# Optimization experiments

Measured on AMD Instinct MI355X. Metric: run time of the kernel, lower is better.

The kernel has to match this reference:

```python
import jax, jax.numpy as jnp
import numpy as np

EMB_DIM = 1024
NUM_HEADS = 16
HEAD_DIM = EMB_DIM // NUM_HEADS
B, S = 4, 2048


def setup_inputs() -> dict:
    key = jax.random.key(0)
    ks = jax.random.split(key, 16)
    def lin(k):
        return jax.random.normal(k, (EMB_DIM, EMB_DIM), jnp.float32) * (EMB_DIM ** -0.5)
    x = jax.random.normal(ks[0], (B, S, EMB_DIM), jnp.float32)
    positions = jnp.sort(jax.random.randint(ks[1], (B, S), 0, 100000), axis=-1)
    return {
        "x": x,
        "positions": positions,
        "Wq": lin(ks[2]), "bq": jnp.zeros((EMB_DIM,), jnp.float32),
        "Wk": lin(ks[3]), "bk": jnp.zeros((EMB_DIM,), jnp.float32),
        "Wv": lin(ks[4]), "bv": jnp.zeros((EMB_DIM,), jnp.float32),
        "Wo": lin(ks[5]), "bo": jnp.zeros((EMB_DIM,), jnp.float32),
        "q_scale": jnp.ones((EMB_DIM,), jnp.float32),
        "k_scale": jnp.ones((EMB_DIM,), jnp.float32),
        "v_scale": jnp.ones((EMB_DIM,), jnp.float32),
        "o_scale": jnp.ones((EMB_DIM,), jnp.float32),
    }


def _rotate(t, cos, sin):
    # t: (B, H, S, D); pairs of consecutive dims rotated by per-position angles.
    # cos/sin: (B, 1, S, D/2)
    tp = t.reshape(t.shape[:-1] + (HEAD_DIM // 2, 2))
    t0, t1 = tp[..., 0], tp[..., 1]
    r0 = t0 * cos - t1 * sin
    r1 = t0 * sin + t1 * cos
    return jnp.stack([r0, r1], axis=-1).reshape(t.shape)


def reference(x, positions, Wq, bq, Wk, bk, Wv, bv, Wo, bo,
              q_scale, k_scale, v_scale, o_scale):
    b, s, e = x.shape
    # theta_vector: standard RoPE inverse frequencies for head_dim
    theta = 1.0 / (10000.0 ** (jnp.arange(0, HEAD_DIM, 2, dtype=jnp.float32) / HEAD_DIM))
    angles = positions.astype(jnp.float32)[..., None] * theta  # (B, S, D/2)
    cos = jnp.cos(angles)[:, None, :, :]  # (B, 1, S, D/2)
    sin = jnp.sin(angles)[:, None, :, :]

    def proj(W, bias, scale):
        y = (x @ W + bias) * scale
        return y.reshape(b, s, NUM_HEADS, HEAD_DIM).transpose(0, 2, 1, 3)  # (B,H,S,D)

    Q = _rotate(proj(Wq, bq, q_scale), cos, sin)
    K = _rotate(proj(Wk, bk, k_scale), cos, sin)
    V = proj(Wv, bv, v_scale)

    scores = jnp.einsum('bhqd,bhkd->bhqk', Q, K) / jnp.sqrt(
        jnp.asarray(HEAD_DIM, jnp.float32))
    probs = jax.nn.softmax(scores, axis=-1)
    context = jnp.einsum('bhqk,bhkd->bhqd', probs, V)
    context = context.transpose(0, 2, 1, 3).reshape(b, s, e)
    return (context @ Wo + bo) * o_scale
```

## Files before the change

kernel.cpp:

```cpp
#include <hip/hip_runtime.h>
#include <hip/hip_bf16.h>

using bf16 = __hip_bfloat16;
typedef __attribute__((ext_vector_type(8))) short short8;
typedef __attribute__((ext_vector_type(4))) float f32x4;
typedef __attribute__((ext_vector_type(16))) float f32x16;

#define AS1 __attribute__((address_space(1)))
#define AS3 __attribute__((address_space(3)))

__device__ __forceinline__ void gload_lds16(const void* g, void* l) {
  __builtin_amdgcn_global_load_lds((const AS1 unsigned int*)g,
                                   (AS3 unsigned int*)l, 16, 0, 0);
}

__device__ __forceinline__ unsigned cvtpk_bf16(float lo, float hi) {
  unsigned r;
  asm("v_cvt_pk_bf16_f32 %0, %1, %2" : "=v"(r) : "v"(lo), "v"(hi));
  return r;
}

__device__ __forceinline__ void pl32swap(unsigned &a, unsigned &b) {
  asm("v_permlane32_swap_b32 %0, %1" : "+v"(a), "+v"(b));
}

__device__ __forceinline__ float fm3(float a, float b, float c) {
  return fmaxf(fmaxf(a, b), c);
}

__global__ __launch_bounds__(256) void k_convert(const float* __restrict__ src,
                                                 bf16* __restrict__ dst, int n4) {
  int i = blockIdx.x * 256 + threadIdx.x;
  if (i >= n4) return;
  float4 v = reinterpret_cast<const float4*>(src)[i];
  alignas(8) bf16 o[4] = {__float2bfloat16(v.x), __float2bfloat16(v.y),
                          __float2bfloat16(v.z), __float2bfloat16(v.w)};
  *reinterpret_cast<uint2*>(dst + (size_t)i * 4) = *reinterpret_cast<uint2*>(o);
}

__global__ __launch_bounds__(256) void k_wtrans(
    const float* __restrict__ W0, const float* __restrict__ W1,
    const float* __restrict__ W2, const float* __restrict__ W3,
    bf16* __restrict__ T0, bf16* __restrict__ T1,
    bf16* __restrict__ T2, bf16* __restrict__ T3) {
  __shared__ float tile[64][65];
  const float* W; bf16* T;
  switch (blockIdx.z) {
    case 0: W = W0; T = T0; break;
    case 1: W = W1; T = T1; break;
    case 2: W = W2; T = T2; break;
    default: W = W3; T = T3; break;
  }
  const int k0 = blockIdx.x * 64, n0 = blockIdx.y * 64;
  const int r = threadIdx.x >> 6, c = threadIdx.x & 63;
#pragma unroll
  for (int i = 0; i < 16; i++)
    tile[r + i * 4][c] = W[(size_t)(k0 + r + i * 4) * 1024 + n0 + c];
  __syncthreads();
#pragma unroll
  for (int i = 0; i < 16; i++)
    T[(size_t)(n0 + r + i * 4) * 1024 + k0 + c] = __float2bfloat16(tile[c][r + i * 4]);
}

__global__ __launch_bounds__(256) void k_gemm_qkv(
    const bf16* __restrict__ A, const bf16* __restrict__ BT,
    const float* __restrict__ bq, const float* __restrict__ bk,
    const float* __restrict__ bv, const float* __restrict__ sq,
    const float* __restrict__ sk, const float* __restrict__ sv,
    bf16* __restrict__ Yqkv) {
  __shared__ alignas(16) bf16 sA[128 * 32];
  __shared__ alignas(16) bf16 sB[128 * 32];
  const int K = 1024;
  const int lane = threadIdx.x & 63;
  const int wid = threadIdx.x >> 6;
  const int wr = wid >> 1, wc = wid & 1;
  const int m0 = blockIdx.x * 128;
  const int n0 = blockIdx.y * 128;

  f32x4 acc[4][4];
#pragma unroll
  for (int i = 0; i < 4; i++)
#pragma unroll
    for (int j = 0; j < 4; j++) acc[i][j] = f32x4{0.f, 0.f, 0.f, 0.f};

  const int srow = lane >> 2;
  const int scol = (lane & 3) * 8;

  for (int k0 = 0; k0 < K; k0 += 32) {
    __syncthreads();
#pragma unroll
    for (int cc = 0; cc < 2; cc++) {
      const int chunk = wid + cc * 4;
      gload_lds16(A + (size_t)(m0 + chunk * 16 + srow) * K + k0 + scol,
                  sA + chunk * 512);
      gload_lds16(BT + (size_t)(n0 + chunk * 16 + srow) * K + k0 + scol,
                  sB + chunk * 512);
    }
    __syncthreads();
    short8 af[4], bfr[4];
#pragma unroll
    for (int i = 0; i < 4; i++) {
      af[i] = *reinterpret_cast<const short8*>(
          sA + (wr * 64 + i * 16 + (lane & 15)) * 32 + (lane >> 4) * 8);
      bfr[i] = *reinterpret_cast<const short8*>(
          sB + (wc * 64 + i * 16 + (lane & 15)) * 32 + (lane >> 4) * 8);
    }
#pragma unroll
    for (int mi = 0; mi < 4; mi++)
#pragma unroll
      for (int ni = 0; ni < 4; ni++)
        acc[mi][ni] = __builtin_amdgcn_mfma_f32_16x16x32_bf16(
            af[mi], bfr[ni], acc[mi][ni], 0, 0, 0);
  }

  const int seg = n0 >> 10;
  bf16* dst = Yqkv + (size_t)seg * (8u << 20);
  const float* bias = seg == 0 ? bq : (seg == 1 ? bk : bv);
  const float* scale = seg == 0 ? sq : (seg == 1 ? sk : sv);
  const int nb = n0 & 1023;
#pragma unroll
  for (int ni = 0; ni < 4; ni++) {
    const int n = nb + wc * 64 + ni * 16 + (lane & 15);
    const float bz = bias[n];
    const float sc = scale[n];
#pragma unroll
    for (int mi = 0; mi < 4; mi++) {
      const int mr = m0 + wr * 64 + mi * 16 + (lane >> 4) * 4;
#pragma unroll
      for (int j = 0; j < 4; j++)
        dst[(size_t)(mr + j) * 1024 + n] = __float2bfloat16((acc[mi][ni][j] + bz) * sc);
    }
  }
}

__global__ __launch_bounds__(256) void k_gemm_bt(
    const bf16* __restrict__ A, const bf16* __restrict__ BT,
    const float* __restrict__ bias, const float* __restrict__ scale,
    float* __restrict__ Cout, int M, int N, int K) {
  __shared__ alignas(16) bf16 sA[128 * 32];
  __shared__ alignas(16) bf16 sB[128 * 32];
  const int lane = threadIdx.x & 63;
  const int wid = threadIdx.x >> 6;
  const int wr = wid >> 1, wc = wid & 1;
  const int m0 = blockIdx.x * 128;
  const int n0 = blockIdx.y * 128;

  f32x4 acc[4][4];
#pragma unroll
  for (int i = 0; i < 4; i++)
#pragma unroll
    for (int j = 0; j < 4; j++) acc[i][j] = f32x4{0.f, 0.f, 0.f, 0.f};

  const int srow = lane >> 2;
  const int scol = (lane & 3) * 8;

  for (int k0 = 0; k0 < K; k0 += 32) {
    __syncthreads();
#pragma unroll
    for (int cc = 0; cc < 2; cc++) {
      const int chunk = wid + cc * 4;
      gload_lds16(A + (size_t)(m0 + chunk * 16 + srow) * K + k0 + scol,
                  sA + chunk * 512);
      gload_lds16(BT + (size_t)(n0 + chunk * 16 + srow) * K + k0 + scol,
                  sB + chunk * 512);
    }
    __syncthreads();
    short8 af[4], bfr[4];
#pragma unroll
    for (int i = 0; i < 4; i++) {
      af[i] = *reinterpret_cast<const short8*>(
          sA + (wr * 64 + i * 16 + (lane & 15)) * 32 + (lane >> 4) * 8);
      bfr[i] = *reinterpret_cast<const short8*>(
          sB + (wc * 64 + i * 16 + (lane & 15)) * 32 + (lane >> 4) * 8);
    }
#pragma unroll
    for (int mi = 0; mi < 4; mi++)
#pragma unroll
      for (int ni = 0; ni < 4; ni++)
        acc[mi][ni] = __builtin_amdgcn_mfma_f32_16x16x32_bf16(
            af[mi], bfr[ni], acc[mi][ni], 0, 0, 0);
  }

#pragma unroll
  for (int ni = 0; ni < 4; ni++) {
    const int n = n0 + wc * 64 + ni * 16 + (lane & 15);
    const float bz = bias[n];
    const float sc = scale[n];
#pragma unroll
    for (int mi = 0; mi < 4; mi++) {
      const int mr = m0 + wr * 64 + mi * 16 + (lane >> 4) * 4;
#pragma unroll
      for (int j = 0; j < 4; j++)
        Cout[(size_t)(mr + j) * N + n] = (acc[mi][ni][j] + bz) * sc;
    }
  }
}

__global__ __launch_bounds__(256) void k_rope(const bf16* __restrict__ Y,
                                              const int* __restrict__ pos,
                                              bf16* __restrict__ Out, float mul) {
  const int idx = blockIdx.x * 256 + threadIdx.x;
  const int c = idx & 3;
  const int h = (idx >> 2) & 15;
  const int s = (idx >> 6) & 2047;
  const int b = idx >> 17;
  const float p = (float)pos[b * 2048 + s];
  const size_t ybase = ((size_t)(b * 2048 + s)) * 1024 + h * 64 + c * 16;
  const size_t obase = (((size_t)(b * 16 + h)) * 2048 + s) * 64 + c * 16;

  union { short8 v[2]; short a[16]; } in, out;
  in.v[0] = *reinterpret_cast<const short8*>(Y + ybase);
  in.v[1] = *reinterpret_cast<const short8*>(Y + ybase + 8);
#pragma unroll
  for (int j = 0; j < 8; j++) {
    const int i = c * 8 + j;
    const float ex = (float)(2 * i) * (1.0f / 64.0f);
    const float theta = 1.0f / powf(10000.0f, ex);
    float sn, cs;
    sincosf(p * theta, &sn, &cs);
    const float f0 = __uint_as_float(((unsigned)(unsigned short)in.a[2 * j]) << 16);
    const float f1 = __uint_as_float(((unsigned)(unsigned short)in.a[2 * j + 1]) << 16);
    out.a[2 * j] = (short)__bfloat16_as_ushort(__float2bfloat16((f0 * cs - f1 * sn) * mul));
    out.a[2 * j + 1] = (short)__bfloat16_as_ushort(__float2bfloat16((f0 * sn + f1 * cs) * mul));
  }
  *reinterpret_cast<short8*>(Out + obase) = out.v[0];
  *reinterpret_cast<short8*>(Out + obase + 8) = out.v[1];
}

__global__ __launch_bounds__(256) void k_vtrans(const bf16* __restrict__ Yv,
                                                bf16* __restrict__ VT) {
  __shared__ bf16 tile[64][66];
  const int s0 = blockIdx.x * 64;
  const int bh = blockIdx.y;
  const int b = bh >> 4, h = bh & 15;
  const int r = threadIdx.x >> 6, c = threadIdx.x & 63;
#pragma unroll
  for (int i = 0; i < 16; i++)
    tile[r + i * 4][c] = Yv[(size_t)(b * 2048 + s0 + r + i * 4) * 1024 + h * 64 + c];
  __syncthreads();
#pragma unroll
  for (int i = 0; i < 16; i++)
    VT[((size_t)bh * 64 + r + i * 4) * 2048 + s0 + c] = tile[c][r + i * 4];
}

__global__ __launch_bounds__(512, 4) void k_attn(const bf16* __restrict__ Q,
                                                 const bf16* __restrict__ Kt,
                                                 const bf16* __restrict__ VT,
                                                 bf16* __restrict__ Ctx) {
  __shared__ alignas(16) bf16 smem[4][4096];

  const int lane = threadIdx.x & 63;
  const int w = threadIdx.x >> 6;
  const int q0 = blockIdx.x * 256;
  const int bh = blockIdx.y;
  const int b = bh >> 4, h = bh & 15;
  const int ql = lane & 31;
  const int hi = lane >> 5;
  const int r8 = lane >> 3;
  const int gslot = (lane & 7) ^ r8;
  const int row_st = w * 8 + r8;

  const bf16* Qrow = Q + ((size_t)bh * 2048 + q0 + w * 32 + ql) * 64;
  short8 qf[4];
#pragma unroll
  for (int ks = 0; ks < 4; ks++)
    qf[ks] = *reinterpret_cast<const short8*>(Qrow + ks * 16 + hi * 8);

  f32x16 accO[2];
#pragma unroll
  for (int dt = 0; dt < 2; dt++)
#pragma unroll
    for (int r = 0; r < 16; r++) accO[dt][r] = 0.f;
  float m = -1e30f, l = 0.f;

  const size_t kbase = (size_t)bh * 2048 * 64;
  const size_t vbase = (size_t)bh * 64 * 2048;

  gload_lds16(Kt + kbase + (size_t)row_st * 64 + gslot * 8, &smem[0][w * 512]);
  gload_lds16(VT + vbase + (size_t)row_st * 2048 + gslot * 8, &smem[2][w * 512]);

  for (int it = 0; it < 32; ++it) {
    __syncthreads();
    const int cur = it & 1;
    if (it + 1 < 32) {
      const int nxt = cur ^ 1, kt = (it + 1) * 64;
      gload_lds16(Kt + kbase + (size_t)(kt + row_st) * 64 + gslot * 8,
                  &smem[nxt][w * 512]);
      gload_lds16(VT + vbase + (size_t)row_st * 2048 + kt + gslot * 8,
                  &smem[2 + nxt][w * 512]);
    }

    f32x16 accS[2];
#pragma unroll
    for (int t = 0; t < 2; t++) {
#pragma unroll
      for (int r = 0; r < 16; r++) accS[t][r] = 0.f;
#pragma unroll
      for (int ks = 0; ks < 4; ks++) {
        const int row = 32 * t + ql;
        const int cs = (2 * ks + hi) ^ (lane & 7);
        short8 kf = *reinterpret_cast<const short8*>(&smem[cur][row * 64 + cs * 8]);
        accS[t] =
            __builtin_amdgcn_mfma_f32_32x32x16_bf16(kf, qf[ks], accS[t], 0, 0, 0);
      }
    }

    float pmax = fmaxf(accS[0][0], accS[0][1]);
#pragma unroll
    for (int r = 2; r < 16; r += 2) pmax = fm3(pmax, accS[0][r], accS[0][r + 1]);
#pragma unroll
    for (int r = 0; r < 16; r += 2) pmax = fm3(pmax, accS[1][r], accS[1][r + 1]);
    pmax = fmaxf(pmax, __shfl_xor(pmax, 32, 64));
    if (__any(pmax - m > 11.0f)) {
      const float mn = fmaxf(m, pmax);
      const float al = exp2f(m - mn);
      m = mn;
      l *= al;
#pragma unroll
      for (int dt = 0; dt < 2; dt++)
#pragma unroll
        for (int r = 0; r < 16; r++) accO[dt][r] *= al;
    }
    float s = 0.f;
#pragma unroll
    for (int t = 0; t < 2; t++)
#pragma unroll
      for (int r = 0; r < 16; r++) {
        const float p = exp2f(accS[t][r] - m);
        accS[t][r] = p;
        s += p;
      }
    s += __shfl_xor(s, 32, 64);
    l += s;

#pragma unroll
    for (int ss = 0; ss < 4; ss++) {
      const int t = ss >> 1, base = (ss & 1) * 8;
      unsigned w01 = cvtpk_bf16(accS[t][base + 0], accS[t][base + 1]);
      unsigned w23 = cvtpk_bf16(accS[t][base + 2], accS[t][base + 3]);
      unsigned w45 = cvtpk_bf16(accS[t][base + 4], accS[t][base + 5]);
      unsigned w67 = cvtpk_bf16(accS[t][base + 6], accS[t][base + 7]);
      pl32swap(w01, w45);
      pl32swap(w23, w67);
      uint4 pau = {w01, w23, w45, w67};
      short8 pa = *reinterpret_cast<short8*>(&pau);
#pragma unroll
      for (int dt = 0; dt < 2; dt++) {
        const int row = 32 * dt + ql;
        const int cs = (2 * ss + hi) ^ (lane & 7);
        short8 vf =
            *reinterpret_cast<const short8*>(&smem[2 + cur][row * 64 + cs * 8]);
        accO[dt] =
            __builtin_amdgcn_mfma_f32_32x32x16_bf16(vf, pa, accO[dt], 0, 0, 0);
      }
    }
  }

  __syncthreads();
  bf16* tw = &smem[0][0] + w * 2048;
  const float inv = 1.0f / l;
#pragma unroll
  for (int dt = 0; dt < 2; dt++)
#pragma unroll
    for (int g = 0; g < 4; g++) {
      unsigned wa = cvtpk_bf16(accO[dt][4 * g + 0] * inv, accO[dt][4 * g + 1] * inv);
      unsigned wb = cvtpk_bf16(accO[dt][4 * g + 2] * inv, accO[dt][4 * g + 3] * inv);
      const int c = (4 * dt + g) ^ (ql & 7);
      uint2 val = {wa, wb};
      *reinterpret_cast<uint2*>(tw + ql * 64 + c * 8 + hi * 4) = val;
    }
  __syncthreads();
  const int qr = lane >> 1, half = lane & 1;
  const size_t orow = (((size_t)b * 2048 + q0 + w * 32 + qr) * 16 + h) * 64;
#pragma unroll
  for (int i = 0; i < 4; i++) {
    const int c2 = (half * 4 + i) ^ (qr & 7);
    short8 v = *reinterpret_cast<const short8*>(tw + qr * 64 + c2 * 8);
    *reinterpret_cast<short8*>(Ctx + orow + half * 32 + i * 8) = v;
  }
}

extern "C" void kernel_launch(void* const* d_in, const int* in_sizes, int n_in,
                              void* d_out, int out_size, void* d_ws, size_t ws_size,
                              hipStream_t stream) {
  const float* x = (const float*)d_in[0];
  const int* positions = (const int*)d_in[1];
  const float* Wq = (const float*)d_in[2];
  const float* bq = (const float*)d_in[3];
  const float* Wk = (const float*)d_in[4];
  const float* bk = (const float*)d_in[5];
  const float* Wv = (const float*)d_in[6];
  const float* bv = (const float*)d_in[7];
  const float* Wo = (const float*)d_in[8];
  const float* bo = (const float*)d_in[9];
  const float* q_scale = (const float*)d_in[10];
  const float* k_scale = (const float*)d_in[11];
  const float* v_scale = (const float*)d_in[12];
  const float* o_scale = (const float*)d_in[13];
  float* out = (float*)d_out;

  char* ws = (char*)d_ws;
  bf16* xb  = (bf16*)(ws);
  bf16* WTq = (bf16*)(ws + (16u << 20));
  bf16* WTk = WTq + (1u << 20);
  bf16* WTv = WTk + (1u << 20);
  bf16* WTo = WTv + (1u << 20);
  bf16* Yq  = (bf16*)(ws + (24u << 20));
  bf16* Yk  = (bf16*)(ws + (40u << 20));
  bf16* Yv  = (bf16*)(ws + (56u << 20));
  bf16* Qr  = xb;
  bf16* Kr  = Yq;
  bf16* VT  = Yk;
  bf16* Ctx = Yv;

  const int M = 8192, N = 1024, K = 1024;

  k_convert<<<8192, 256, 0, stream>>>(x, xb, M * K / 4);
  k_wtrans<<<dim3(16, 16, 4), 256, 0, stream>>>(Wq, Wk, Wv, Wo, WTq, WTk, WTv, WTo);

  k_gemm_qkv<<<dim3(64, 24), 256, 0, stream>>>(xb, WTq, bq, bk, bv,
                                               q_scale, k_scale, v_scale, Yq);

  k_rope<<<2048, 256, 0, stream>>>(Yq, positions, Qr, 0.18033688011112042f);
  k_rope<<<2048, 256, 0, stream>>>(Yk, positions, Kr, 1.0f);
  k_vtrans<<<dim3(32, 64), 256, 0, stream>>>(Yv, VT);

  k_attn<<<dim3(8, 64), 512, 0, stream>>>(Qr, Kr, VT, Ctx);

  k_gemm_bt<<<dim3(64, 8), 256, 0, stream>>>(Ctx, WTo, bo, o_scale, out, M, N, K);
}
```

Measured before the change: 378.9 us.

## Double-buffer LDS tiles in GEMMs and reorder attention grid dimensions

Both GEMM kernels now keep two LDS stages, issuing the next K-tile's global-to-LDS loads before computing on the current one. This drops one barrier per iteration and overlaps memory latency with MFMA work, at the cost of doubled LDS per block. The attention launch swaps grid axes so blocks for the same head are no longer adjacent in dispatch order, which changes which blocks run together and how they share K/V in cache. The double-buffer relies on the single barrier plus the implicit wait for the async LDS loads before the fragment reads, so correctness depends on how the compiler inserts vmcnt waits.

```diff
diff --git a/kernel.cpp b/kernel.cpp
--- a/kernel.cpp
+++ b/kernel.cpp
@@ -68,8 +68,8 @@
     const float* __restrict__ bv, const float* __restrict__ sq,
     const float* __restrict__ sk, const float* __restrict__ sv,
     bf16* __restrict__ Yqkv) {
-  __shared__ alignas(16) bf16 sA[128 * 32];
-  __shared__ alignas(16) bf16 sB[128 * 32];
+  __shared__ alignas(16) bf16 sA[2][4096];
+  __shared__ alignas(16) bf16 sB[2][4096];
   const int K = 1024;
   const int lane = threadIdx.x & 63;
   const int wid = threadIdx.x >> 6;
@@ -86,24 +86,34 @@
   const int srow = lane >> 2;
   const int scol = (lane & 3) * 8;
 
-  for (int k0 = 0; k0 < K; k0 += 32) {
+#pragma unroll
+  for (int cc = 0; cc < 2; cc++) {
+    const int chunk = wid + cc * 4;
+    gload_lds16(A + (size_t)(m0 + chunk * 16 + srow) * K + scol, &sA[0][chunk * 512]);
+    gload_lds16(BT + (size_t)(n0 + chunk * 16 + srow) * K + scol, &sB[0][chunk * 512]);
+  }
+
+  for (int kt = 0; kt < 32; kt++) {
     __syncthreads();
-#pragma unroll
-    for (int cc = 0; cc < 2; cc++) {
-      const int chunk = wid + cc * 4;
-      gload_lds16(A + (size_t)(m0 + chunk * 16 + srow) * K + k0 + scol,
-                  sA + chunk * 512);
-      gload_lds16(BT + (size_t)(n0 + chunk * 16 + srow) * K + k0 + scol,
-                  sB + chunk * 512);
-    }
-    __syncthreads();
+    const int cur = kt & 1;
+    if (kt + 1 < 32) {
+      const int nxt = cur ^ 1, k0 = (kt + 1) * 32;
+#pragma unroll
+      for (int cc = 0; cc < 2; cc++) {
+        const int chunk = wid + cc * 4;
+        gload_lds16(A + (size_t)(m0 + chunk * 16 + srow) * K + k0 + scol,
+                    &sA[nxt][chunk * 512]);
+        gload_lds16(BT + (size_t)(n0 + chunk * 16 + srow) * K + k0 + scol,
+                    &sB[nxt][chunk * 512]);
+      }
+    }
     short8 af[4], bfr[4];
 #pragma unroll
     for (int i = 0; i < 4; i++) {
       af[i] = *reinterpret_cast<const short8*>(
-          sA + (wr * 64 + i * 16 + (lane & 15)) * 32 + (lane >> 4) * 8);
+          &sA[cur][(wr * 64 + i * 16 + (lane & 15)) * 32 + (lane >> 4) * 8]);
       bfr[i] = *reinterpret_cast<const short8*>(
-          sB + (wc * 64 + i * 16 + (lane & 15)) * 32 + (lane >> 4) * 8);
+          &sB[cur][(wc * 64 + i * 16 + (lane & 15)) * 32 + (lane >> 4) * 8]);
     }
 #pragma unroll
     for (int mi = 0; mi < 4; mi++)
@@ -137,13 +147,14 @@
     const bf16* __restrict__ A, const bf16* __restrict__ BT,
     const float* __restrict__ bias, const float* __restrict__ scale,
     float* __restrict__ Cout, int M, int N, int K) {
-  __shared__ alignas(16) bf16 sA[128 * 32];
-  __shared__ alignas(16) bf16 sB[128 * 32];
+  __shared__ alignas(16) bf16 sA[2][4096];
+  __shared__ alignas(16) bf16 sB[2][4096];
   const int lane = threadIdx.x & 63;
   const int wid = threadIdx.x >> 6;
   const int wr = wid >> 1, wc = wid & 1;
   const int m0 = blockIdx.x * 128;
   const int n0 = blockIdx.y * 128;
+  const int NT = K >> 5;
 
   f32x4 acc[4][4];
 #pragma unroll
@@ -154,24 +165,34 @@
   const int srow = lane >> 2;
   const int scol = (lane & 3) * 8;
 
-  for (int k0 = 0; k0 < K; k0 += 32) {
+#pragma unroll
+  for (int cc = 0; cc < 2; cc++) {
+    const int chunk = wid + cc * 4;
+    gload_lds16(A + (size_t)(m0 + chunk * 16 + srow) * K + scol, &sA[0][chunk * 512]);
+    gload_lds16(BT + (size_t)(n0 + chunk * 16 + srow) * K + scol, &sB[0][chunk * 512]);
+  }
+
+  for (int kt = 0; kt < NT; kt++) {
     __syncthreads();
-#pragma unroll
-    for (int cc = 0; cc < 2; cc++) {
-      const int chunk = wid + cc * 4;
-      gload_lds16(A + (size_t)(m0 + chunk * 16 + srow) * K + k0 + scol,
-                  sA + chunk * 512);
-      gload_lds16(BT + (size_t)(n0 + chunk * 16 + srow) * K + k0 + scol,
-                  sB + chunk * 512);
-    }
-    __syncthreads();
+    const int cur = kt & 1;
+    if (kt + 1 < NT) {
+      const int nxt = cur ^ 1, k0 = (kt + 1) * 32;
+#pragma unroll
+      for (int cc = 0; cc < 2; cc++) {
+        const int chunk = wid + cc * 4;
+        gload_lds16(A + (size_t)(m0 + chunk * 16 + srow) * K + k0 + scol,
+                    &sA[nxt][chunk * 512]);
+        gload_lds16(BT + (size_t)(n0 + chunk * 16 + srow) * K + k0 + scol,
+                    &sB[nxt][chunk * 512]);
+      }
+    }
     short8 af[4], bfr[4];
 #pragma unroll
     for (int i = 0; i < 4; i++) {
       af[i] = *reinterpret_cast<const short8*>(
-          sA + (wr * 64 + i * 16 + (lane & 15)) * 32 + (lane >> 4) * 8);
+          &sA[cur][(wr * 64 + i * 16 + (lane & 15)) * 32 + (lane >> 4) * 8]);
       bfr[i] = *reinterpret_cast<const short8*>(
-          sB + (wc * 64 + i * 16 + (lane & 15)) * 32 + (lane >> 4) * 8);
+          &sB[cur][(wc * 64 + i * 16 + (lane & 15)) * 32 + (lane >> 4) * 8]);
     }
 #pragma unroll
     for (int mi = 0; mi < 4; mi++)
@@ -251,8 +272,8 @@
 
   const int lane = threadIdx.x & 63;
   const int w = threadIdx.x >> 6;
-  const int q0 = blockIdx.x * 256;
-  const int bh = blockIdx.y;
+  const int bh = blockIdx.x;
+  const int q0 = blockIdx.y * 256;
   const int b = bh >> 4, h = bh & 15;
   const int ql = lane & 31;
   const int hi = lane >> 5;
@@ -425,7 +446,7 @@
   k_rope<<<2048, 256, 0, stream>>>(Yk, positions, Kr, 1.0f);
   k_vtrans<<<dim3(32, 64), 256, 0, stream>>>(Yv, VT);
 
-  k_attn<<<dim3(8, 64), 512, 0, stream>>>(Qr, Kr, VT, Ctx);
+  k_attn<<<dim3(64, 8), 512, 0, stream>>>(Qr, Kr, VT, Ctx);
 
   k_gemm_bt<<<dim3(64, 8), 256, 0, stream>>>(Ctx, WTo, bo, o_scale, out, M, N, K);
 }
```

New measurement: 381.4 us. No clear change (+0.7%).
